# Kernel optimization log

Measured on AMD Instinct MI355X. Metric: run time of the kernel, lower is better.

The kernel has to match this reference:

```python
import jax, jax.numpy as jnp
import numpy as np

# Static conv config (matches init_kwargs)
STRIDE = (1, 1, 1)
PAD = (1, 1, 1)
DIL = (1, 1, 1)
DG = 1  # deformable groups


def setup_inputs() -> dict:
    key = jax.random.key(0)
    k1, k2, k3 = jax.random.split(key, 3)
    N, Cin, T, H, W = 2, 32, 8, 56, 56
    Cout, kT, kH, kW = 64, 3, 3, 3
    x = jax.random.normal(k1, (N, Cin, T, H, W), dtype=jnp.float32)
    # offset channels = DG * 3 * kT*kH*kW = 81 ; layout [N, dg*K*3, To, Ho, Wo]
    offset = jax.random.normal(k2, (N, DG * 3 * kT * kH * kW, T, H, W), dtype=jnp.float32)
    stdv = 1.0 / np.sqrt(Cin * kT * kH * kW)
    weight = jax.random.uniform(k3, (Cout, Cin, kT, kH, kW), dtype=jnp.float32, minval=-stdv, maxval=stdv)
    bias = jnp.zeros((Cout,), dtype=jnp.float32)
    return {"x": x, "offset": offset, "weight": weight, "bias": bias}


def _deform_conv3d(x, offset, weight, bias):
    N, C, T, H, W = x.shape
    Co, _, kT, kH, kW = weight.shape
    K = kT * kH * kW
    st, sh, sw = STRIDE
    pt_, ph_, pw_ = PAD
    dt_, dh_, dw_ = DIL
    To = (T + 2 * pt_ - (dt_ * (kT - 1) + 1)) // st + 1
    Ho = (H + 2 * ph_ - (dh_ * (kH - 1) + 1)) // sh + 1
    Wo = (W + 2 * pw_ - (dw_ * (kW - 1) + 1)) // sw + 1
    Cg = C // DG
    # offsets: [N, DG, K, 3(dt,dh,dw), To, Ho, Wo]
    off = offset.reshape(N, DG, K, 3, To, Ho, Wo)
    kt, kh, kw = [g.reshape(-1) for g in jnp.meshgrid(
        jnp.arange(kT), jnp.arange(kH), jnp.arange(kW), indexing='ij')]
    # base sampling grid per kernel tap: [K, To, Ho, Wo] via broadcasting
    bt = (jnp.arange(To) * st - pt_)[None, :, None, None] + (kt * dt_)[:, None, None, None]
    bh = (jnp.arange(Ho) * sh - ph_)[None, None, :, None] + (kh * dh_)[:, None, None, None]
    bw = (jnp.arange(Wo) * sw - pw_)[None, None, None, :] + (kw * dw_)[:, None, None, None]
    # fractional sampling positions: [N, DG, K, To, Ho, Wo]
    pt = bt[None, None] + off[:, :, :, 0]
    ph = bh[None, None] + off[:, :, :, 1]
    pw = bw[None, None] + off[:, :, :, 2]
    t0f, h0f, w0f = jnp.floor(pt), jnp.floor(ph), jnp.floor(pw)
    lt, lh, lw = pt - t0f, ph - h0f, pw - w0f
    t0 = t0f.astype(jnp.int32)
    h0 = h0f.astype(jnp.int32)
    w0 = w0f.astype(jnp.int32)
    x_flat = x.reshape(N, DG, Cg, T * H * W)
    acc = jnp.zeros((N, DG, Cg, K, To, Ho, Wo), dtype=x.dtype)
    for ct in (0, 1):
        ti = t0 + ct
        wt = lt if ct else (1.0 - lt)
        for ch in (0, 1):
            hi = h0 + ch
            wh = lh if ch else (1.0 - lh)
            for cw in (0, 1):
                wi = w0 + cw
                ww = lw if cw else (1.0 - lw)
                valid = ((ti >= 0) & (ti < T) & (hi >= 0) & (hi < H) & (wi >= 0) & (wi < W))
                idx = (jnp.clip(ti, 0, T - 1) * H + jnp.clip(hi, 0, H - 1)) * W + jnp.clip(wi, 0, W - 1)
                v = jnp.take_along_axis(x_flat, idx.reshape(N, DG, 1, -1), axis=3)
                v = v.reshape(N, DG, Cg, K, To, Ho, Wo)
                wgt = (wt * wh * ww * valid.astype(x.dtype))[:, :, None]  # [N,DG,1,K,To,Ho,Wo]
                acc = acc + v * wgt
    w_r = weight.reshape(Co, DG, Cg, K)
    out = jnp.einsum('ogck,ngcktuv->notuv', w_r, acc)
    if bias.size > 0:
        out = out + bias[None, :, None, None, None]
    return out


def reference(x, offset, weight, bias):
    return _deform_conv3d(x, offset, weight, bias)
```

## Files before the change

### kernel.cpp

```cpp
#include <hip/hip_runtime.h>
#include <hip/hip_fp16.h>

#define CIN   32
#define COUT  64
#define TT    8
#define HH    56
#define WW    56
#define KK    27
#define SP    (TT * HH * WW)
#define NB    2
#define NBLK  784
#define KSPLIT 14

typedef __attribute__((ext_vector_type(8))) _Float16 half8;
typedef __attribute__((ext_vector_type(4))) float    f32x4;

#define WF_OFF   0
#define XTH_OFF  (128 << 10)

__global__ __launch_bounds__(256) void prep_kernel(const float* __restrict__ x,
                                                   const float* __restrict__ w,
                                                   __half* __restrict__ xTh,
                                                   __half* __restrict__ wf) {
    const int b = blockIdx.x;
    const int t = threadIdx.x;
    if (b < NBLK) {
        __shared__ float sm[CIN][65];
        const int s0 = b * 64, n = s0 / SP, sp0 = s0 % SP;
#pragma unroll
        for (int it = 0; it < 8; ++it) {
            const int idx = it * 256 + t, c = idx >> 6, l = idx & 63;
            sm[c][l] = x[((size_t)n * CIN + c) * SP + sp0 + l];
        }
        __syncthreads();
#pragma unroll
        for (int it = 0; it < 4; ++it) {
            const int idx = it * 256 + t, l = idx >> 4, cp = idx & 15;
            ((__half2*)xTh)[((size_t)n * SP + sp0 + l) * (CIN / 2) + cp] =
                __floats2half2_rn(sm[2 * cp][l], sm[2 * cp + 1][l]);
        }
    } else {
        const int k = b - NBLK;
#pragma unroll
        for (int it = 0; it < 8; ++it) {
            const int idx  = it * 256 + t;
            const int j    = idx & 7;
            const int lane = (idx >> 3) & 63;
            const int ct   = (idx >> 9) & 3;
            const int co   = ct * 16 + (lane & 15);
            const int c    = (lane >> 4) * 8 + j;
            wf[(((size_t)k * 4 + ct) * 64 + lane) * 8 + j] =
                __float2half(w[((size_t)co * CIN + c) * KK + k]);
        }
    }
}

__global__ __launch_bounds__(512, 6) void dconv3d_kernel(const __half* __restrict__ xTh,
                                                         const float* __restrict__ off,
                                                         const __half* __restrict__ wf,
                                                         const float* __restrict__ bias,
                                                         float* __restrict__ out) {
    __shared__ __align__(16) char smem[81 * 64 * 4];
    float (*offs)[64] = reinterpret_cast<float(*)[64]>(smem);
    float (*cmb)[4][64] = reinterpret_cast<float(*)[4][64]>(smem);

    const int t    = threadIdx.x;
    const int lane = t & 63;
    const int wv   = t >> 6;
    const int wpos = wv & 3;
    const int half = wv >> 2;

    const int posI = lane >> 2;
    const int cgI  = lane & 3;
    const int jg   = lane >> 4;

    const int bp_addr = (((lane & 15) << 2) | jg) << 2;

    const int sb  = (blockIdx.x & 7) * 98 + (blockIdx.x >> 3);
    const int s0  = sb * 64;
    const int n   = s0 / SP;
    const int spb = s0 % SP;

    {
        const float* offbase = off + ((size_t)n * (3 * KK)) * SP + spb;
        for (int i = t; i < 81 * 16; i += 512) {
            const int row = i >> 4, q = i & 15;
            *(float4*)&offs[row][q * 4] = *(const float4*)(offbase + (size_t)row * SP + q * 4);
        }
    }
    __syncthreads();

    const int sp = spb + wpos * 16 + posI;
    const int to = sp / (HH * WW);
    const int hw = sp % (HH * WW);
    const int ho = hw / WW;
    const int wo = hw % WW;
    const int pl = wpos * 16 + posI;

    f32x4 acc[4];
#pragma unroll
    for (int ct = 0; ct < 4; ++ct)
#pragma unroll
        for (int r = 0; r < 4; ++r)
            acc[ct][r] = half ? 0.f : bias[ct * 16 + jg * 4 + r];

    const __half* xn = xTh + (size_t)n * SP * CIN;

    auto tap = [&](int k) {
        const int kt  = k / 9;
        const int khh = (k / 3) % 3;
        const int kww = k % 3;

        const float pt_ = (float)(to - 1 + kt)  + offs[k * 3 + 0][pl];
        const float ph_ = (float)(ho - 1 + khh) + offs[k * 3 + 1][pl];
        const float pw_ = (float)(wo - 1 + kww) + offs[k * 3 + 2][pl];

        const float ft = floorf(pt_), fh = floorf(ph_), fw = floorf(pw_);
        const float lt = pt_ - ft, lh = ph_ - fh, lw = pw_ - fw;
        const int t0 = (int)ft, h0 = (int)fh, w0 = (int)fw;
        const int t1 = t0 + 1, h1 = h0 + 1, w1 = w0 + 1;

        float awt[2], awh[2], aww[2];
        int   it2[2], ih2[2], iw2[2];
        awt[0] = (t0 >= 0 && t0 < TT) ? (1.f - lt) : 0.f;
        awt[1] = (t1 >= 0 && t1 < TT) ? lt : 0.f;
        it2[0] = min(max(t0, 0), TT - 1);  it2[1] = min(max(t1, 0), TT - 1);
        awh[0] = (h0 >= 0 && h0 < HH) ? (1.f - lh) : 0.f;
        awh[1] = (h1 >= 0 && h1 < HH) ? lh : 0.f;
        ih2[0] = min(max(h0, 0), HH - 1);  ih2[1] = min(max(h1, 0), HH - 1);
        aww[0] = (w0 >= 0 && w0 < WW) ? (1.f - lw) : 0.f;
        aww[1] = (w1 >= 0 && w1 < WW) ? lw : 0.f;
        iw2[0] = min(max(w0, 0), WW - 1);  iw2[1] = min(max(w1, 0), WW - 1);

        int   a[8];
        float cw[8];
#pragma unroll
        for (int ci = 0; ci < 8; ++ci) {
            const int i0 = ci >> 2, i1 = (ci >> 1) & 1, i2 = ci & 1;
            a[ci]  = (it2[i0] * HH + ih2[i1]) * WW + iw2[i2];
            cw[ci] = awt[i0] * awh[i1] * aww[i2];
        }

        float4 g[8];
#pragma unroll
        for (int ci = 0; ci < 8; ++ci)
            g[ci] = *(const float4*)(xn + (size_t)a[ci] * CIN + cgI * 8);

        __half2 vacc[4];
#pragma unroll
        for (int j = 0; j < 4; ++j) vacc[j] = __floats2half2_rn(0.f, 0.f);
#pragma unroll
        for (int ci = 0; ci < 8; ++ci) {
            const __half2* uh = (const __half2*)&g[ci];
            const __half2 cw2 = __float2half2_rn(cw[ci]);
            vacc[0] = __hfma2(cw2, uh[0], vacc[0]);
            vacc[1] = __hfma2(cw2, uh[1], vacc[1]);
            vacc[2] = __hfma2(cw2, uh[2], vacc[2]);
            vacc[3] = __hfma2(cw2, uh[3], vacc[3]);
        }

        union { __half2 h2[4]; int i[4]; half8 h8; } u, v;
#pragma unroll
        for (int d = 0; d < 4; ++d) u.h2[d] = vacc[d];
#pragma unroll
        for (int d = 0; d < 4; ++d)
            v.i[d] = __builtin_amdgcn_ds_bpermute(bp_addr, u.i[d]);
        const half8 bfrag = v.h8;

#pragma unroll
        for (int ct = 0; ct < 4; ++ct) {
            const half8 af = *(const half8*)(wf + (((size_t)k * 4 + ct) * 64 + lane) * 8);
            acc[ct] = __builtin_amdgcn_mfma_f32_16x16x32_f16(af, bfrag, acc[ct], 0, 0, 0);
        }
    };

    if (half == 0) {
#pragma unroll 2
        for (int k = 0; k < KSPLIT; ++k) tap(k);
    } else {
#pragma unroll 2
        for (int k = KSPLIT; k < KK; ++k) tap(k);
    }

    __syncthreads();
    if (half == 1) {
#pragma unroll
        for (int ct = 0; ct < 4; ++ct)
#pragma unroll
            for (int r = 0; r < 4; ++r) cmb[ct * 4 + r][wpos][lane] = acc[ct][r];
    }
    __syncthreads();
    if (half == 0) {
#pragma unroll
        for (int ct = 0; ct < 4; ++ct)
#pragma unroll
            for (int r = 0; r < 4; ++r) {
                const int co = ct * 16 + jg * 4 + r;
                out[((size_t)n * COUT + co) * SP + spb + wpos * 16 + (lane & 15)] =
                    acc[ct][r] + cmb[ct * 4 + r][wpos][lane];
            }
    }
}

extern "C" void kernel_launch(void* const* d_in, const int* in_sizes, int n_in,
                              void* d_out, int out_size, void* d_ws, size_t ws_size,
                              hipStream_t stream) {
    const float* x    = (const float*)d_in[0];
    const float* off  = (const float*)d_in[1];
    const float* w    = (const float*)d_in[2];
    const float* bias = (const float*)d_in[3];
    float* out        = (float*)d_out;

    __half* wf  = (__half*)((char*)d_ws + WF_OFF);
    __half* xTh = (__half*)((char*)d_ws + XTH_OFF);

    prep_kernel<<<NBLK + KK, 256, 0, stream>>>(x, w, xTh, wf);
    dconv3d_kernel<<<NBLK, 512, 0, stream>>>(xTh, off, wf, bias, out);
}
```

Measured before the change: 124.4 us.

## Split kernel taps four ways across waves with 32-position blocks

Each block now covers 32 output positions instead of 64, and its 8 waves split the 27 kernel taps into four groups (7/7/7/6) instead of two halves. Partial accumulators from the three non-leading groups are combined through shared memory before the store. The grid doubles to 1568 blocks and launch bounds ask for 8 blocks per SM, aiming for more parallelism and better latency hiding on the gather loads. In exchange it adds a larger shared-memory reduction and repeats the bias and offset setup per block, and the 'unroll 2' hint on the tap loop is dropped.

```diff
diff --git a/kernel.cpp b/kernel.cpp
--- a/kernel.cpp
+++ b/kernel.cpp
@@ -9,8 +9,9 @@
 #define KK    27
 #define SP    (TT * HH * WW)
 #define NB    2
-#define NBLK  784
-#define KSPLIT 14
+#define POSB  32
+#define NBLK  ((NB * SP) / POSB)
+#define NBLKP 784
 
 typedef __attribute__((ext_vector_type(8))) _Float16 half8;
 typedef __attribute__((ext_vector_type(4))) float    f32x4;
@@ -24,7 +25,7 @@
                                                    __half* __restrict__ wf) {
     const int b = blockIdx.x;
     const int t = threadIdx.x;
-    if (b < NBLK) {
+    if (b < NBLKP) {
         __shared__ float sm[CIN][65];
         const int s0 = b * 64, n = s0 / SP, sp0 = s0 % SP;
 #pragma unroll
@@ -40,7 +41,7 @@
                 __floats2half2_rn(sm[2 * cp][l], sm[2 * cp + 1][l]);
         }
     } else {
-        const int k = b - NBLK;
+        const int k = b - NBLKP;
 #pragma unroll
         for (int it = 0; it < 8; ++it) {
             const int idx  = it * 256 + t;
@@ -55,20 +56,20 @@
     }
 }
 
-__global__ __launch_bounds__(512, 6) void dconv3d_kernel(const __half* __restrict__ xTh,
+__global__ __launch_bounds__(512, 8) void dconv3d_kernel(const __half* __restrict__ xTh,
                                                          const float* __restrict__ off,
                                                          const __half* __restrict__ wf,
                                                          const float* __restrict__ bias,
                                                          float* __restrict__ out) {
-    __shared__ __align__(16) char smem[81 * 64 * 4];
-    float (*offs)[64] = reinterpret_cast<float(*)[64]>(smem);
-    float (*cmb)[4][64] = reinterpret_cast<float(*)[4][64]>(smem);
+    __shared__ __align__(16) char smem[3 * 16 * 2 * 64 * 4];
+    float (*offs)[POSB] = reinterpret_cast<float(*)[POSB]>(smem);
+    float (*cmb)[16][2][64] = reinterpret_cast<float(*)[16][2][64]>(smem);
 
     const int t    = threadIdx.x;
     const int lane = t & 63;
     const int wv   = t >> 6;
-    const int wpos = wv & 3;
-    const int half = wv >> 2;
+    const int wpos = wv & 1;
+    const int q    = wv >> 1;
 
     const int posI = lane >> 2;
     const int cgI  = lane & 3;
@@ -76,37 +77,40 @@
 
     const int bp_addr = (((lane & 15) << 2) | jg) << 2;
 
-    const int sb  = (blockIdx.x & 7) * 98 + (blockIdx.x >> 3);
-    const int s0  = sb * 64;
+    const int sb  = (blockIdx.x & 7) * 196 + (blockIdx.x >> 3);
+    const int s0  = sb * POSB;
     const int n   = s0 / SP;
     const int spb = s0 % SP;
 
     {
         const float* offbase = off + ((size_t)n * (3 * KK)) * SP + spb;
-        for (int i = t; i < 81 * 16; i += 512) {
-            const int row = i >> 4, q = i & 15;
-            *(float4*)&offs[row][q * 4] = *(const float4*)(offbase + (size_t)row * SP + q * 4);
+        for (int i = t; i < 81 * 8; i += 512) {
+            const int row = i >> 3, qd = i & 7;
+            *(float4*)&offs[row][qd * 4] = *(const float4*)(offbase + (size_t)row * SP + qd * 4);
         }
     }
     __syncthreads();
 
-    const int sp = spb + wpos * 16 + posI;
+    const int pl = wpos * 16 + posI;
+    const int sp = spb + pl;
     const int to = sp / (HH * WW);
     const int hw = sp % (HH * WW);
     const int ho = hw / WW;
     const int wo = hw % WW;
-    const int pl = wpos * 16 + posI;
 
     f32x4 acc[4];
 #pragma unroll
     for (int ct = 0; ct < 4; ++ct)
 #pragma unroll
         for (int r = 0; r < 4; ++r)
-            acc[ct][r] = half ? 0.f : bias[ct * 16 + jg * 4 + r];
+            acc[ct][r] = q ? 0.f : bias[ct * 16 + jg * 4 + r];
 
     const __half* xn = xTh + (size_t)n * SP * CIN;
 
-    auto tap = [&](int k) {
+    const int kbeg = q * 7;
+    const int kend = (q == 3) ? KK : kbeg + 7;
+
+    for (int k = kbeg; k < kend; ++k) {
         const int kt  = k / 9;
         const int khh = (k / 3) % 3;
         const int kww = k % 3;
@@ -172,32 +176,27 @@
             const half8 af = *(const half8*)(wf + (((size_t)k * 4 + ct) * 64 + lane) * 8);
             acc[ct] = __builtin_amdgcn_mfma_f32_16x16x32_f16(af, bfrag, acc[ct], 0, 0, 0);
         }
-    };
-
-    if (half == 0) {
-#pragma unroll 2
-        for (int k = 0; k < KSPLIT; ++k) tap(k);
-    } else {
-#pragma unroll 2
-        for (int k = KSPLIT; k < KK; ++k) tap(k);
     }
 
     __syncthreads();
-    if (half == 1) {
+    if (q != 0) {
 #pragma unroll
         for (int ct = 0; ct < 4; ++ct)
 #pragma unroll
-            for (int r = 0; r < 4; ++r) cmb[ct * 4 + r][wpos][lane] = acc[ct][r];
+            for (int r = 0; r < 4; ++r)
+                cmb[q - 1][ct * 4 + r][wpos][lane] = acc[ct][r];
     }
     __syncthreads();
-    if (half == 0) {
+    if (q == 0) {
 #pragma unroll
         for (int ct = 0; ct < 4; ++ct)
 #pragma unroll
             for (int r = 0; r < 4; ++r) {
                 const int co = ct * 16 + jg * 4 + r;
-                out[((size_t)n * COUT + co) * SP + spb + wpos * 16 + (lane & 15)] =
-                    acc[ct][r] + cmb[ct * 4 + r][wpos][lane];
+                float v = acc[ct][r];
+#pragma unroll
+                for (int j = 0; j < 3; ++j) v += cmb[j][ct * 4 + r][wpos][lane];
+                out[((size_t)n * COUT + co) * SP + spb + wpos * 16 + (lane & 15)] = v;
             }
     }
 }
@@ -214,6 +213,6 @@
     __half* wf  = (__half*)((char*)d_ws + WF_OFF);
     __half* xTh = (__half*)((char*)d_ws + XTH_OFF);
 
-    prep_kernel<<<NBLK + KK, 256, 0, stream>>>(x, w, xTh, wf);
+    prep_kernel<<<NBLKP + KK, 256, 0, stream>>>(x, w, xTh, wf);
     dconv3d_kernel<<<NBLK, 512, 0, stream>>>(xTh, off, wf, bias, out);
 }
```

Result: no change. 125.7 us (+1.1%).
